# Kernel optimization log

Measured on AMD Instinct MI355X. Metric: run time of the kernel, lower is better.

## Reference

```python
import jax, jax.numpy as jnp
import numpy as np

DELTA = 0.1
LOSS_WEIGHT = 1.0


def setup_inputs() -> dict:
    key = jax.random.key(0)
    k1, k2 = jax.random.split(key)
    N, D = 4000000, 4
    pred = jax.random.normal(k1, (N, D), dtype=jnp.float32)
    target = jax.random.normal(k2, (N, D), dtype=jnp.float32)
    return {"pred": pred, "target": target}


def _ssim_loss_mean(pred, target):
    # Per-row SSIM. diag(mm(A, B.T)) == sum(A * B, axis=1), so the O(N^2)
    # torch.mm + diag collapses to a single-pass O(N*D) row reduction.
    D = pred.shape[1]
    mean_pred = jnp.mean(pred, axis=1, keepdims=True)    # [N, 1]
    mean_target = jnp.mean(target, axis=1, keepdims=True)
    dp = pred - mean_pred
    dt = target - mean_target
    inv = 1.0 / (D - 1)
    var_pred = jnp.sum(dp * dp, axis=1, keepdims=True) * inv
    var_target = jnp.sum(dt * dt, axis=1, keepdims=True) * inv
    cov = jnp.sum(dp * dt, axis=1, keepdims=True) * inv
    a1 = 2.0 * mean_pred * mean_target + DELTA
    a2 = 2.0 * cov + DELTA
    b1 = mean_pred ** 2 + mean_target ** 2 + DELTA
    b2 = var_pred + var_target + DELTA
    similar = a1 * a2 / (b1 * b2 + DELTA)
    loss = 1.0 - similar                                  # [N, 1]
    return jnp.mean(loss)                                 # reduction='mean'


def reference(pred, target):
    loss = LOSS_WEIGHT * _ssim_loss_mean(pred, target)
    # NaN fallback from the original forward:
    # ones_like(target).sum() / (N * D) == 1.0, computed faithfully.
    nan_flag = (jnp.isnan(loss)
                | jnp.any(jnp.isnan(pred))
                | jnp.any(jnp.isnan(target)))
    n_elem = target.shape[0] * target.shape[1]
    fallback = jnp.sum(jnp.ones_like(target)) / n_elem
    return jnp.where(nan_flag, fallback, loss)
```

## Files before the change

### kernel.cpp

```cpp
#include <hip/hip_runtime.h>
#include <math.h>

#define DELTA 0.1f

__global__ __launch_bounds__(256) void ssim_loss_kernel(
    const float4* __restrict__ pred,
    const float4* __restrict__ target,
    double* __restrict__ accum,
    int N)
{
    int tid = blockIdx.x * blockDim.x + threadIdx.x;
    int stride = gridDim.x * blockDim.x;

    float local = 0.0f;
    for (int i = tid; i < N; i += stride) {
        float4 p = pred[i];
        float4 t = target[i];

        float mp = (p.x + p.y + p.z + p.w) * 0.25f;
        float mt = (t.x + t.y + t.z + t.w) * 0.25f;

        float dpx = p.x - mp, dpy = p.y - mp, dpz = p.z - mp, dpw = p.w - mp;
        float dtx = t.x - mt, dty = t.y - mt, dtz = t.z - mt, dtw = t.w - mt;

        const float inv = 1.0f / 3.0f;
        float vp  = (dpx*dpx + dpy*dpy + dpz*dpz + dpw*dpw) * inv;
        float vt  = (dtx*dtx + dty*dty + dtz*dtz + dtw*dtw) * inv;
        float cov = (dpx*dtx + dpy*dty + dpz*dtz + dpw*dtw) * inv;

        float a1 = 2.0f * mp * mt + DELTA;
        float a2 = 2.0f * cov + DELTA;
        float b1 = mp * mp + mt * mt + DELTA;
        float b2 = vp + vt + DELTA;

        float similar = (a1 * a2) / (b1 * b2 + DELTA);
        local += 1.0f - similar;
    }

    #pragma unroll
    for (int off = 32; off > 0; off >>= 1)
        local += __shfl_down(local, off, 64);

    __shared__ float wave_sums[4];
    int lane = threadIdx.x & 63;
    int wid  = threadIdx.x >> 6;
    if (lane == 0) wave_sums[wid] = local;
    __syncthreads();

    if (threadIdx.x == 0) {
        float s = wave_sums[0] + wave_sums[1] + wave_sums[2] + wave_sums[3];
        atomicAdd(accum, (double)s);
    }
}

__global__ void ssim_finalize_kernel(const double* __restrict__ accum,
                                     float* __restrict__ out, int N)
{
    double mean = *accum / (double)N;
    float f = (float)mean;
    if (isnan(f)) f = 1.0f;
    *out = f;
}

extern "C" void kernel_launch(void* const* d_in, const int* in_sizes, int n_in,
                              void* d_out, int out_size, void* d_ws, size_t ws_size,
                              hipStream_t stream)
{
    const float4* pred   = (const float4*)d_in[0];
    const float4* target = (const float4*)d_in[1];
    int N = in_sizes[0] / 4;

    double* accum = (double*)d_ws;
    hipMemsetAsync(d_ws, 0, sizeof(double), stream);

    const int block = 256;
    const int grid  = 2048;
    ssim_loss_kernel<<<grid, block, 0, stream>>>(pred, target, accum, N);
    ssim_finalize_kernel<<<1, 1, 0, stream>>>(accum, (float*)d_out, N);
}
```

Measured before the change: 159.5 us.

## Batch row loads per thread and fuse finalize via last-block counter

Each thread now issues five independent float4 loads per input before computing, so more memory requests are in flight. The grid is sized so each thread covers about five rows instead of using a fixed 2048-block grid-stride loop. The separate finalize kernel is removed: the last block to finish, detected with an atomic counter, writes the mean, which saves one launch. This costs more registers per thread and a longer atomic tail.

```diff
diff --git a/kernel.cpp b/kernel.cpp
--- a/kernel.cpp
+++ b/kernel.cpp
@@ -2,46 +2,60 @@
 #include <math.h>
 
 #define DELTA 0.1f
+constexpr int BLOCK = 256;
+constexpr int RPT   = 5;
 
-__global__ __launch_bounds__(256) void ssim_loss_kernel(
+__device__ __forceinline__ float row_loss(float4 p, float4 t) {
+    float mp = (p.x + p.y + p.z + p.w) * 0.25f;
+    float mt = (t.x + t.y + t.z + t.w) * 0.25f;
+    float dpx = p.x - mp, dpy = p.y - mp, dpz = p.z - mp, dpw = p.w - mp;
+    float dtx = t.x - mt, dty = t.y - mt, dtz = t.z - mt, dtw = t.w - mt;
+    const float inv = 1.0f / 3.0f;
+    float vp  = (dpx*dpx + dpy*dpy + dpz*dpz + dpw*dpw) * inv;
+    float vt  = (dtx*dtx + dty*dty + dtz*dtz + dtw*dtw) * inv;
+    float cov = (dpx*dtx + dpy*dty + dpz*dtz + dpw*dtw) * inv;
+    float a1 = 2.0f * mp * mt + DELTA;
+    float a2 = 2.0f * cov + DELTA;
+    float b1 = mp * mp + mt * mt + DELTA;
+    float b2 = vp + vt + DELTA;
+    return 1.0f - (a1 * a2) / (b1 * b2 + DELTA);
+}
+
+__global__ __launch_bounds__(BLOCK, 8) void ssim_loss_kernel(
     const float4* __restrict__ pred,
     const float4* __restrict__ target,
     double* __restrict__ accum,
+    unsigned int* __restrict__ counter,
+    float* __restrict__ out,
     int N)
 {
-    int tid = blockIdx.x * blockDim.x + threadIdx.x;
-    int stride = gridDim.x * blockDim.x;
+    const int S    = gridDim.x * BLOCK;
+    const int gtid = blockIdx.x * BLOCK + threadIdx.x;
 
     float local = 0.0f;
-    for (int i = tid; i < N; i += stride) {
-        float4 p = pred[i];
-        float4 t = target[i];
 
-        float mp = (p.x + p.y + p.z + p.w) * 0.25f;
-        float mt = (t.x + t.y + t.z + t.w) * 0.25f;
-
-        float dpx = p.x - mp, dpy = p.y - mp, dpz = p.z - mp, dpw = p.w - mp;
-        float dtx = t.x - mt, dty = t.y - mt, dtz = t.z - mt, dtw = t.w - mt;
-
-        const float inv = 1.0f / 3.0f;
-        float vp  = (dpx*dpx + dpy*dpy + dpz*dpz + dpw*dpw) * inv;
-        float vt  = (dtx*dtx + dty*dty + dtz*dtz + dtw*dtw) * inv;
-        float cov = (dpx*dtx + dpy*dty + dpz*dtz + dpw*dtw) * inv;
-
-        float a1 = 2.0f * mp * mt + DELTA;
-        float a2 = 2.0f * cov + DELTA;
-        float b1 = mp * mp + mt * mt + DELTA;
-        float b2 = vp + vt + DELTA;
-
-        float similar = (a1 * a2) / (b1 * b2 + DELTA);
-        local += 1.0f - similar;
+    if (RPT * S <= N) {
+        float4 p[RPT], t[RPT];
+        #pragma unroll
+        for (int k = 0; k < RPT; ++k) {
+            p[k] = pred[gtid + k * S];
+            t[k] = target[gtid + k * S];
+        }
+        #pragma unroll
+        for (int k = 0; k < RPT; ++k)
+            local += row_loss(p[k], t[k]);
+        for (int i = RPT * S + gtid; i < N; i += S)
+            local += row_loss(pred[i], target[i]);
+    } else {
+        for (int i = gtid; i < N; i += S)
+            local += row_loss(pred[i], target[i]);
     }
 
     #pragma unroll
     for (int off = 32; off > 0; off >>= 1)
         local += __shfl_down(local, off, 64);
 
-    __shared__ float wave_sums[4];
+    __shared__ float wave_sums[BLOCK / 64];
     int lane = threadIdx.x & 63;
     int wid  = threadIdx.x >> 6;
     if (lane == 0) wave_sums[wid] = local;
@@ -50,16 +64,16 @@
     if (threadIdx.x == 0) {
         float s = wave_sums[0] + wave_sums[1] + wave_sums[2] + wave_sums[3];
         atomicAdd(accum, (double)s);
+        __threadfence();
+        unsigned int done = atomicAdd(counter, 1u);
+        if (done == gridDim.x - 1) {
+            __threadfence();
+            double total = atomicAdd(accum, 0.0);
+            float f = (float)(total / (double)N);
+            if (isnan(f)) f = 1.0f;
+            *out = f;
+        }
     }
-}
-
-__global__ void ssim_finalize_kernel(const double* __restrict__ accum,
-                                     float* __restrict__ out, int N)
-{
-    double mean = *accum / (double)N;
-    float f = (float)mean;
-    if (isnan(f)) f = 1.0f;
-    *out = f;
 }
 
 extern "C" void kernel_launch(void* const* d_in, const int* in_sizes, int n_in,
@@ -68,13 +82,14 @@
 {
     const float4* pred   = (const float4*)d_in[0];
     const float4* target = (const float4*)d_in[1];
-    int N = in_sizes[0] / 4;
+    int rows = in_sizes[0] / 4;
 
-    double* accum = (double*)d_ws;
-    hipMemsetAsync(d_ws, 0, sizeof(double), stream);
+    double*       accum   = (double*)d_ws;
+    unsigned int* counter = (unsigned int*)((char*)d_ws + 8);
+    hipMemsetAsync(d_ws, 0, 16, stream);
 
-    const int block = 256;
-    const int grid  = 2048;
-    ssim_loss_kernel<<<grid, block, 0, stream>>>(pred, target, accum, N);
-    ssim_finalize_kernel<<<1, 1, 0, stream>>>(accum, (float*)d_out, N);
+    int grid = rows / (BLOCK * RPT);
+    if (grid < 1) grid = 1;
+    ssim_loss_kernel<<<grid, BLOCK, 0, stream>>>(pred, target, accum, counter,
+                                                 (float*)d_out, rows);
 }
```

Result: slower. 286.6 us (+79.6%).
